# Optimization experiments

Measured on AMD Instinct MI355X. Metric: run time of the kernel, lower is better.

## Reference

```python
import jax, jax.numpy as jnp
import numpy as np

G = 16          # num graphs (equal-size contiguous segments)
P = 500         # kde_grid_points
Q = 20          # num quantiles, np.linspace(0,1,20)
SQRT2PI = float(np.sqrt(2.0 * np.pi))


def _gcn(x, src, dst, W, b):
    # PyG GCNConv: add self-loops, symmetric D^-1/2 (A+I) D^-1/2 aggregation.
    N = x.shape[0]
    xw = x @ W
    deg = jax.ops.segment_sum(jnp.ones_like(src, dtype=x.dtype), dst, num_segments=N) + 1.0
    dinv = jax.lax.rsqrt(deg)
    msg = xw[src] * (dinv[src] * dinv[dst])[:, None]            # [E, D]
    agg = jax.ops.segment_sum(msg, dst, num_segments=N) + xw * (dinv * dinv)[:, None]
    return agg + b


def _att_pool(x, Wg, bg):
    # GlobalAttention: softmax(gate_nn(x)) per graph, weighted sum of x.
    xg = x.reshape(G, -1, x.shape[-1])                          # [G, n, D]
    a = jax.nn.softmax(xg @ Wg + bg, axis=1)                    # [G, n, 1]
    return jnp.sum(a * xg, axis=1)                              # [G, D]


def _kde(xg):
    # xg: [n, D] nodes of one graph -> [D*Q] soft quantile features.
    quant = jnp.linspace(0.0, 1.0, Q, dtype=xg.dtype)
    n = xg.shape[0]
    mn = xg.min(axis=0) - 1e-6
    mx = xg.max(axis=0) + 1e-6
    grid = jnp.linspace(0.0, 1.0, P, dtype=xg.dtype)[:, None] * (mx - mn) + mn   # [P, D]
    std = xg.std(axis=0) + 1e-8 / 3                              # unbiased=False
    h = 1.06 * std * n ** (-0.2)                                 # Silverman bandwidth
    u = (grid[:, None, :] - xg[None, :, :]) / h                  # [P, n, D]
    kern = jnp.exp(-0.5 * u * u) / (h * SQRT2PI)
    dens = kern.mean(axis=1)                                     # [P, D]
    cdf = jnp.cumsum(dens, axis=0)
    cdf = cdf / jnp.clip(cdf[-1:], 1e-8)
    dist = jnp.abs(cdf[:, :, None] - quant)                      # [P, D, Q]
    w = jax.nn.sigmoid(-100.0 * dist)
    w = w / (w.sum(axis=0, keepdims=True) + 1e-8)
    return jnp.sum(grid[:, :, None] * w, axis=0).reshape(-1)     # [D*Q]


def setup_inputs() -> dict:
    key = jax.random.key(0)
    ks = jax.random.split(key, 26)
    N, E, D_in, D_h, D_out = 2048, 32768, 64, 64, 16
    rn = lambda k, s: jax.random.normal(k, s, jnp.float32) * 0.1
    return {
        'x': jax.random.normal(ks[0], (N, D_in), jnp.float32),
        'edge_index': jax.random.randint(ks[1], (2, E), 0, N),
        'gcn_W0': rn(ks[2], (D_in, D_h)), 'gcn_b0': rn(ks[3], (D_h,)),
        'gcn_W1': rn(ks[4], (D_h, D_h)), 'gcn_b1': rn(ks[5], (D_h,)),
        'lp_W0': rn(ks[6], (D_in, D_out)), 'lp_b0': rn(ks[7], (D_out,)),
        'lp_W1': rn(ks[8], (D_h, D_out)), 'lp_b1': rn(ks[9], (D_out,)),
        'cls_W': rn(ks[10], (D_h, D_out)), 'cls_b': rn(ks[11], (D_out,)),
        'kp_W0': rn(ks[12], (D_in * Q, D_out)), 'kp_b0': rn(ks[13], (D_out,)),
        'kp_W1': rn(ks[14], (D_h * Q, D_out)), 'kp_b1': rn(ks[15], (D_out,)),
        'gate_W0': rn(ks[16], (D_in, 1)), 'gate_b0': rn(ks[17], (1,)),
        'gate_W1': rn(ks[18], (D_h, 1)), 'gate_b1': rn(ks[19], (1,)),
        'gate_W2': rn(ks[20], (D_h, 1)), 'gate_b2': rn(ks[21], (1,)),
        'beta': jax.random.normal(ks[22], (D_out,), jnp.float32),
        'h0': jax.random.normal(ks[23], (1,), jnp.float32),
    }


def reference(x, edge_index, gcn_W0, gcn_b0, gcn_W1, gcn_b1, lp_W0, lp_b0, lp_W1, lp_b1,
              cls_W, cls_b, kp_W0, kp_b0, kp_W1, kp_b1, gate_W0, gate_b0, gate_W1, gate_b1,
              gate_W2, gate_b2, beta, h0):
    src, dst = edge_index[0], edge_index[1]
    gcn_p = [(gcn_W0, gcn_b0), (gcn_W1, gcn_b1)]
    lp = [(lp_W0, lp_b0), (lp_W1, lp_b1)]
    kp = [(kp_W0, kp_b0), (kp_W1, kp_b1)]
    gate = [(gate_W0, gate_b0), (gate_W1, gate_b1)]
    cur = x
    h_list, kde_list = [], []
    for i in range(2):  # n_layers (dropout is identity in eval)
        pooled = _att_pool(cur, *gate[i])                        # [G, D]
        h_list.append(pooled @ lp[i][0] + lp[i][1])              # [G, out]
        kf = jax.vmap(_kde)(cur.reshape(G, -1, cur.shape[-1]))   # [G, D*Q]
        kde_list.append(kf @ kp[i][0] + kp[i][1])
        cur = _gcn(cur, src, dst, *gcn_p[i])
    h_list.append(_att_pool(cur, gate_W2, gate_b2) @ cls_W + cls_b)
    main_out = jnp.stack(h_list).mean(axis=0)                    # [G, out]
    kde_out = jnp.stack(kde_list).mean(axis=0)
    return (main_out + kde_out) @ beta + h0                      # [G]
```

## Files before the change

kernel.cpp:

```cpp
#include <hip/hip_runtime.h>
#include <math.h>

#define NNODE 2048
#define NEDGE 32768
#define DD 64
#define GG 16
#define NPG 128
#define PP 500
#define QQ 20
#define CAP 64

__device__ __forceinline__ float fexp2(float x) { return __builtin_amdgcn_exp2f(x); }
__device__ __forceinline__ float frcp(float x)  { return __builtin_amdgcn_rcpf(x); }
__device__ __forceinline__ float frsq(float x)  { return __builtin_amdgcn_rsqf(x); }

struct __align__(8) f2 { float x, y; };

struct KdeS { f2 bc[NPG]; f2 cg[512]; float sred[8]; float wtot[8]; float kfv[QQ]; };
struct AttS { float sc[NPG]; float part[8][DD]; float pooled[DD]; };
struct XwS  { float Ws[DD][DD]; float xr[8][DD]; };
union SmemU { KdeS k; AttS a; XwS x; };

__global__ void k_zero(int* __restrict__ p) {
    p[blockIdx.x * 512 + threadIdx.x] = 0;
}

__global__ void k_fill(const int* __restrict__ ei, int* __restrict__ cnt,
                       int* __restrict__ csr) {
    int e = blockIdx.x * 256 + threadIdx.x;
    int s = ei[e], dstn = ei[NEDGE + e];
    int pos = atomicAdd(&cnt[dstn], 1);
    if (pos < CAP) csr[dstn * CAP + pos] = s;
}

__device__ __forceinline__ void att_pool(AttS& s, const float* __restrict__ xg,
                                         const float* __restrict__ gW, float gb) {
    int t = threadIdx.x, lane = t & 63, wid = t >> 6;
    int node = t >> 2, seg = t & 3;
    const float* row = xg + node * DD + seg * 16;
    const float* gw = gW + seg * 16;
    float v = 0.f;
    #pragma unroll
    for (int k = 0; k < 16; k++) v = fmaf(row[k], gw[k], v);
    v += __shfl_xor(v, 1);
    v += __shfl_xor(v, 2);
    if (seg == 0) s.sc[node] = v + gb;
    __syncthreads();
    if (wid == 0) {
        float v0 = s.sc[lane], v1 = s.sc[lane + 64];
        float m = fmaxf(v0, v1);
        for (int o = 32; o; o >>= 1) m = fmaxf(m, __shfl_xor(m, o));
        float e0 = __expf(v0 - m), e1 = __expf(v1 - m);
        float ssum = e0 + e1;
        for (int o = 32; o; o >>= 1) ssum += __shfl_xor(ssum, o);
        float inv = frcp(ssum);
        s.sc[lane] = e0 * inv;
        s.sc[lane + 64] = e1 * inv;
    }
    __syncthreads();
    int d2 = t & 63, ch = t >> 6;
    const float* base = xg + ch * 16 * DD + d2;
    const float* av = s.sc + ch * 16;
    float p = 0.f;
    #pragma unroll
    for (int i = 0; i < 16; i++) p = fmaf(av[i], base[i * DD], p);
    s.part[ch][d2] = p;
    __syncthreads();
    if (t < DD) {
        float pd = 0.f;
        #pragma unroll
        for (int c2 = 0; c2 < 8; c2++) pd += s.part[c2][t];
        s.pooled[t] = pd;
    }
    __syncthreads();
}

__global__ __launch_bounds__(512) void k_mega(
    const float* __restrict__ xin, const int* __restrict__ cnt,
    float* __restrict__ xwout, float* __restrict__ hb, float* __restrict__ kpart,
    const float* __restrict__ gcnW,
    const float* __restrict__ gateW, const float* __restrict__ gateB,
    const float* __restrict__ lpW, const float* __restrict__ lpB,
    const float* __restrict__ kpW) {
    __shared__ SmemU sm;
    int b = blockIdx.x, t = threadIdx.x, lane = t & 63, wid = t >> 6;

    if (b < GG * DD) {
        int g = b >> 6, d = b & 63;
        const float* xg = xin + g * NPG * DD + d;
        float a = 0.f;
        if (t < NPG) a = xg[t * DD];
        if (wid < 2) {
            float mn = a, mx = a, smv = a;
            for (int o = 32; o; o >>= 1) {
                mn = fminf(mn, __shfl_xor(mn, o));
                mx = fmaxf(mx, __shfl_xor(mx, o));
                smv += __shfl_xor(smv, o);
            }
            if (lane == 0) {
                sm.k.sred[wid * 3 + 0] = mn;
                sm.k.sred[wid * 3 + 1] = mx;
                sm.k.sred[wid * 3 + 2] = smv;
            }
        }
        __syncthreads();
        float mn = fminf(sm.k.sred[0], sm.k.sred[3]) - 1e-6f;
        float mx = fmaxf(sm.k.sred[1], sm.k.sred[4]) + 1e-6f;
        float mean = (sm.k.sred[2] + sm.k.sred[5]) * (1.f / 128.f);
        if (wid < 2) {
            float dv = a - mean;
            float sq = dv * dv;
            for (int o = 32; o; o >>= 1) sq += __shfl_xor(sq, o);
            if (lane == 0) sm.k.sred[6 + wid] = sq;
        }
        __syncthreads();
        float var = fmaxf((sm.k.sred[6] + sm.k.sred[7]) * (1.f / 128.f), 0.f);
        float sd = sqrtf(var) + (1e-8f / 3.0f);
        float h = 0.4016648901252554f * sd;
        const float L2E = 1.4426950408889634f;
        float A = -0.5f * L2E * frcp(h * h);
        if (t < NPG) { f2 v; v.x = -2.f * A * a; v.y = A * a * a; sm.k.bc[t] = v; }
        __syncthreads();
        float step = (mx - mn) * (1.f / 499.f);
        float gp = fmaf(step, (float)t, mn);
        float gA = A * gp * gp;
        const float4* bc4 = (const float4*)sm.k.bc;
        float ac0 = 0.f, ac1 = 0.f, ac2 = 0.f, ac3 = 0.f;
        #pragma unroll 4
        for (int j4 = 0; j4 < 64; j4 += 2) {
            float4 p = bc4[j4], q = bc4[j4 + 1];
            ac0 += fexp2(gA + fmaf(p.x, gp, p.y));
            ac1 += fexp2(gA + fmaf(p.z, gp, p.w));
            ac2 += fexp2(gA + fmaf(q.x, gp, q.y));
            ac3 += fexp2(gA + fmaf(q.z, gp, q.w));
        }
        float invnh = frcp(128.f * h * 2.5066282746310002f);
        float dens = (t < PP) ? ((ac0 + ac1) + (ac2 + ac3)) * invnh : 0.f;
        float sc2 = dens;
        for (int o = 1; o < 64; o <<= 1) {
            float u = __shfl_up(sc2, o);
            if (lane >= o) sc2 += u;
        }
        if (lane == 63) sm.k.wtot[wid] = sc2;
        __syncthreads();
        float offs = 0.f, total = 0.f;
        #pragma unroll
        for (int w = 0; w < 8; w++) {
            float wv = sm.k.wtot[w];
            if (w < wid) offs += wv;
            total += wv;
        }
        float c = (offs + sc2) * frcp(fmaxf(total, 1e-8f));
        f2 cgv; cgv.x = (t < PP) ? c : 4.0f; cgv.y = (t < PP) ? gp : 0.f;
        sm.k.cg[t] = cgv;
        __syncthreads();
        int grp = t >> 4, sub = t & 15;
        if (grp < QQ) {
            float qv = (float)grp * (1.f / 19.f);
            float sw0 = 0.f, sw1 = 0.f, sg0 = 0.f, sg1 = 0.f;
            #pragma unroll
            for (int i = 0; i < 32; i += 2) {
                f2 v0 = sm.k.cg[i * 16 + sub];
                f2 v1 = sm.k.cg[(i + 1) * 16 + sub];
                float e0 = fexp2(fabsf(v0.x - qv) * 144.26950408889634f);
                float e1 = fexp2(fabsf(v1.x - qv) * 144.26950408889634f);
                float w0 = frcp(1.f + e0), w1 = frcp(1.f + e1);
                sw0 += w0; sg0 = fmaf(w0, v0.y, sg0);
                sw1 += w1; sg1 = fmaf(w1, v1.y, sg1);
            }
            float sw = sw0 + sw1, sg = sg0 + sg1;
            #pragma unroll
            for (int o = 1; o < 16; o <<= 1) {
                sw += __shfl_xor(sw, o);
                sg += __shfl_xor(sg, o);
            }
            if (sub == 0) sm.k.kfv[grp] = sg * frcp(sw + 1e-8f);
        }
        __syncthreads();
        if (t < 16) {
            float v = 0.f;
            #pragma unroll
            for (int q = 0; q < QQ; q++) v = fmaf(sm.k.kfv[q], kpW[(d * QQ + q) * 16 + t], v);
            kpart[b * 16 + t] = v;
        }
    } else if (b < GG * DD + GG) {
        int g = b - GG * DD;
        att_pool(sm.a, xin + g * NPG * DD, gateW, gateB[0]);
        if (t < 16) {
            float o = lpB[t];
            #pragma unroll
            for (int d2 = 0; d2 < DD; d2++) o = fmaf(sm.a.pooled[d2], lpW[d2 * 16 + t], o);
            hb[g * 16 + t] = o;
        }
    } else {
        int rb = b - (GG * DD + GG);
        int r0 = rb * 8;
        float4* Wv = (float4*)&sm.x.Ws[0][0];
        const float4* Gv = (const float4*)gcnW;
        Wv[t] = Gv[t];
        Wv[t + 512] = Gv[t + 512];
        sm.x.xr[wid][lane] = xin[(r0 + wid) * DD + lane];
        __syncthreads();
        float s = 0.f;
        #pragma unroll
        for (int k = 0; k < DD; k++) s = fmaf(sm.x.xr[wid][k], sm.x.Ws[k][lane], s);
        float di = frsq((float)cnt[r0 + wid] + 1.0f);
        xwout[(r0 + wid) * DD + lane] = s * di;
    }
}

__global__ __launch_bounds__(512) void k_gather(const int* __restrict__ cnt,
                                                const int* __restrict__ csr,
                                                const float* __restrict__ xw,
                                                const float* __restrict__ bvec,
                                                float* __restrict__ cur) {
    int t = threadIdx.x, lane = t & 63, wid = t >> 6;
    int n = blockIdx.x * 8 + wid;
    int ec = cnt[n];
    if (ec > CAP) ec = CAP;
    const int* lst = csr + n * CAP;
    float sum0 = 0.f, sum1 = 0.f;
    int j = 0;
    for (; j + 4 <= ec; j += 4) {
        int s0 = lst[j], s1 = lst[j + 1], s2 = lst[j + 2], s3 = lst[j + 3];
        sum0 += xw[s0 * DD + lane] + xw[s1 * DD + lane];
        sum1 += xw[s2 * DD + lane] + xw[s3 * DD + lane];
    }
    for (; j < ec; j++) sum0 += xw[lst[j] * DD + lane];
    float di = frsq((float)cnt[n] + 1.f);
    cur[n * DD + lane] = di * ((sum0 + sum1) + xw[n * DD + lane]) + bvec[lane];
}

__global__ __launch_bounds__(512) void k_fin(const float* __restrict__ cur2,
    const float* __restrict__ gW2, const float* __restrict__ gb2,
    const float* __restrict__ clsW, const float* __restrict__ clsB,
    const float* __restrict__ hb, const float* __restrict__ kpart,
    const float* __restrict__ kpb0, const float* __restrict__ kpb1,
    const float* __restrict__ beta, const float* __restrict__ h0s,
    float* __restrict__ out) {
    __shared__ SmemU sm;
    __shared__ float red[16];
    int g = blockIdx.x, t = threadIdx.x;
    att_pool(sm.a, cur2 + g * NPG * DD, gW2, gb2[0]);
    if (t < 16) {
        float h2 = clsB[t];
        #pragma unroll
        for (int d2 = 0; d2 < DD; d2++) h2 = fmaf(sm.a.pooled[d2], clsW[d2 * 16 + t], h2);
        const float* kp0 = kpart + g * DD * 16 + t;
        const float* kp1 = kp0 + GG * DD * 16;
        float s0 = 0.f, s1 = 0.f;
        #pragma unroll
        for (int d2 = 0; d2 < DD; d2++) {
            s0 += kp0[d2 * 16];
            s1 += kp1[d2 * 16];
        }
        float mo = (hb[g * 16 + t] + hb[256 + g * 16 + t] + h2) * (1.f / 3.f);
        float ko = (s0 + kpb0[t] + s1 + kpb1[t]) * 0.5f;
        red[t] = (mo + ko) * beta[t];
    }
    __syncthreads();
    if (t == 0) {
        float s = 0.f;
        #pragma unroll
        for (int j = 0; j < 16; j++) s += red[j];
        out[g] = s + h0s[0];
    }
}

extern "C" void kernel_launch(void* const* d_in, const int* in_sizes, int n_in,
                              void* d_out, int out_size, void* d_ws, size_t ws_size,
                              hipStream_t stream) {
    const float* x       = (const float*)d_in[0];
    const int*   ei      = (const int*)  d_in[1];
    const float* gcn_W0  = (const float*)d_in[2];
    const float* gcn_b0  = (const float*)d_in[3];
    const float* gcn_W1  = (const float*)d_in[4];
    const float* gcn_b1  = (const float*)d_in[5];
    const float* lp_W0   = (const float*)d_in[6];
    const float* lp_b0   = (const float*)d_in[7];
    const float* lp_W1   = (const float*)d_in[8];
    const float* lp_b1   = (const float*)d_in[9];
    const float* cls_W   = (const float*)d_in[10];
    const float* cls_b   = (const float*)d_in[11];
    const float* kp_W0   = (const float*)d_in[12];
    const float* kp_b0   = (const float*)d_in[13];
    const float* kp_W1   = (const float*)d_in[14];
    const float* kp_b1   = (const float*)d_in[15];
    const float* gate_W0 = (const float*)d_in[16];
    const float* gate_b0 = (const float*)d_in[17];
    const float* gate_W1 = (const float*)d_in[18];
    const float* gate_b1 = (const float*)d_in[19];
    const float* gate_W2 = (const float*)d_in[20];
    const float* gate_b2 = (const float*)d_in[21];
    const float* beta    = (const float*)d_in[22];
    const float* h0s     = (const float*)d_in[23];

    float* ws  = (float*)d_ws;
    int* cnt   = (int*)ws;
    int* csr   = (int*)(ws + 2048);
    float* A   = ws + 2048 + NNODE * CAP;
    float* B   = A + NNODE * DD;
    float* hb  = B + NNODE * DD;
    float* kp  = hb + 512;

    k_zero<<<4, 512, 0, stream>>>(cnt);

    k_fill<<<NEDGE / 256, 256, 0, stream>>>(ei, cnt, csr);

    k_mega<<<GG * DD + GG + NNODE / 8, 512, 0, stream>>>(
        x, cnt, A, hb, kp, gcn_W0, gate_W0, gate_b0, lp_W0, lp_b0, kp_W0);
    k_gather<<<NNODE / 8, 512, 0, stream>>>(cnt, csr, A, gcn_b0, B);

    k_mega<<<GG * DD + GG + NNODE / 8, 512, 0, stream>>>(
        B, cnt, A, hb + 256, kp + GG * DD * 16, gcn_W1, gate_W1, gate_b1, lp_W1, lp_b1, kp_W1);
    k_gather<<<NNODE / 8, 512, 0, stream>>>(cnt, csr, A, gcn_b1, B);

    k_fin<<<GG, 512, 0, stream>>>(B, gate_W2, gate_b2, cls_W, cls_b,
                                  hb, kp, kp_b0, kp_b1, beta, h0s, (float*)d_out);
}
```

Before: 66.45 us.

## Fuse all stages into one persistent cooperative kernel with grid syncs

Replaces the seven separate launches (zero, CSR fill, two mega, two gather, final) with a single cooperative kernel of 256 blocks. Stages are separated by grid.sync, and one block builds the CSR while the other 255 run the layer-0 KDE, pooling and xW units. Because xW is now computed before the degree counts exist, the source-side degree scaling moves into the gather, which reads cnt[src] per edge. This removes launch gaps but serializes the CSR build onto one block and runs about six work units per block in the compute phases.

Result: slower. 241.1 us (+262.8%).

```diff
diff --git a/kernel.cpp b/kernel.cpp
--- a/kernel.cpp
+++ b/kernel.cpp
@@ -1,5 +1,8 @@
 #include <hip/hip_runtime.h>
+#include <hip/hip_cooperative_groups.h>
 #include <math.h>
+
+namespace cg = cooperative_groups;
 
 #define NNODE 2048
 #define NEDGE 32768
@@ -9,6 +12,8 @@
 #define PP 500
 #define QQ 20
 #define CAP 64
+#define NBLK 256
+#define NCOMP (NBLK - 1)
 
 __device__ __forceinline__ float fexp2(float x) { return __builtin_amdgcn_exp2f(x); }
 __device__ __forceinline__ float frcp(float x)  { return __builtin_amdgcn_rcpf(x); }
@@ -21,17 +26,17 @@
 struct XwS  { float Ws[DD][DD]; float xr[8][DD]; };
 union SmemU { KdeS k; AttS a; XwS x; };
 
-__global__ void k_zero(int* __restrict__ p) {
-    p[blockIdx.x * 512 + threadIdx.x] = 0;
-}
-
-__global__ void k_fill(const int* __restrict__ ei, int* __restrict__ cnt,
-                       int* __restrict__ csr) {
-    int e = blockIdx.x * 256 + threadIdx.x;
-    int s = ei[e], dstn = ei[NEDGE + e];
-    int pos = atomicAdd(&cnt[dstn], 1);
-    if (pos < CAP) csr[dstn * CAP + pos] = s;
-}
+struct Params {
+    const float *x; const int *ei;
+    const float *gcn_W0, *gcn_b0, *gcn_W1, *gcn_b1;
+    const float *lp_W0, *lp_b0, *lp_W1, *lp_b1;
+    const float *cls_W, *cls_b;
+    const float *kp_W0, *kp_b0, *kp_W1, *kp_b1;
+    const float *gate_W0, *gate_b0, *gate_W1, *gate_b1, *gate_W2, *gate_b2;
+    const float *beta, *h0s;
+    int *cnt, *csr;
+    float *A, *B, *hb, *kpart, *out;
+};
 
 __device__ __forceinline__ void att_pool(AttS& s, const float* __restrict__ xg,
                                          const float* __restrict__ gW, float gb) {
@@ -75,18 +80,18 @@
     __syncthreads();
 }
 
-__global__ __launch_bounds__(512) void k_mega(
-    const float* __restrict__ xin, const int* __restrict__ cnt,
-    float* __restrict__ xwout, float* __restrict__ hb, float* __restrict__ kpart,
+__device__ void mega_unit(SmemU& sm, int vb,
+    const float* __restrict__ xin,
+    float* __restrict__ xwout, float* __restrict__ hbL, float* __restrict__ kpartL,
     const float* __restrict__ gcnW,
     const float* __restrict__ gateW, const float* __restrict__ gateB,
     const float* __restrict__ lpW, const float* __restrict__ lpB,
     const float* __restrict__ kpW) {
-    __shared__ SmemU sm;
-    int b = blockIdx.x, t = threadIdx.x, lane = t & 63, wid = t >> 6;
-
-    if (b < GG * DD) {
-        int g = b >> 6, d = b & 63;
+    int t = threadIdx.x, lane = t & 63, wid = t >> 6;
+    __syncthreads();
+
+    if (vb < GG * DD) {
+        int g = vb >> 6, d = vb & 63;
         const float* xg = xin + g * NPG * DD + d;
         float a = 0.f;
         if (t < NPG) a = xg[t * DD];
@@ -117,8 +122,7 @@
         float var = fmaxf((sm.k.sred[6] + sm.k.sred[7]) * (1.f / 128.f), 0.f);
         float sd = sqrtf(var) + (1e-8f / 3.0f);
         float h = 0.4016648901252554f * sd;
-        const float L2E = 1.4426950408889634f;
-        float A = -0.5f * L2E * frcp(h * h);
+        float A = -0.5f * 1.4426950408889634f * frcp(h * h);
         if (t < NPG) { f2 v; v.x = -2.f * A * a; v.y = A * a * a; sm.k.bc[t] = v; }
         __syncthreads();
         float step = (mx - mn) * (1.f / 499.f);
@@ -181,19 +185,19 @@
             float v = 0.f;
             #pragma unroll
             for (int q = 0; q < QQ; q++) v = fmaf(sm.k.kfv[q], kpW[(d * QQ + q) * 16 + t], v);
-            kpart[b * 16 + t] = v;
-        }
-    } else if (b < GG * DD + GG) {
-        int g = b - GG * DD;
+            kpartL[vb * 16 + t] = v;
+        }
+    } else if (vb < GG * DD + GG) {
+        int g = vb - GG * DD;
         att_pool(sm.a, xin + g * NPG * DD, gateW, gateB[0]);
         if (t < 16) {
             float o = lpB[t];
             #pragma unroll
             for (int d2 = 0; d2 < DD; d2++) o = fmaf(sm.a.pooled[d2], lpW[d2 * 16 + t], o);
-            hb[g * 16 + t] = o;
+            hbL[g * 16 + t] = o;
         }
     } else {
-        int rb = b - (GG * DD + GG);
+        int rb = vb - (GG * DD + GG);
         int r0 = rb * 8;
         float4* Wv = (float4*)&sm.x.Ws[0][0];
         const float4* Gv = (const float4*)gcnW;
@@ -204,117 +208,144 @@
         float s = 0.f;
         #pragma unroll
         for (int k = 0; k < DD; k++) s = fmaf(sm.x.xr[wid][k], sm.x.Ws[k][lane], s);
-        float di = frsq((float)cnt[r0 + wid] + 1.0f);
-        xwout[(r0 + wid) * DD + lane] = s * di;
-    }
-}
-
-__global__ __launch_bounds__(512) void k_gather(const int* __restrict__ cnt,
-                                                const int* __restrict__ csr,
-                                                const float* __restrict__ xw,
-                                                const float* __restrict__ bvec,
-                                                float* __restrict__ cur) {
+        xwout[(r0 + wid) * DD + lane] = s;
+    }
+}
+
+__device__ void gather_unit(const int* __restrict__ cnt, const int* __restrict__ csr,
+                            const float* __restrict__ xw, const float* __restrict__ bvec,
+                            float* __restrict__ cur) {
     int t = threadIdx.x, lane = t & 63, wid = t >> 6;
     int n = blockIdx.x * 8 + wid;
-    int ec = cnt[n];
-    if (ec > CAP) ec = CAP;
+    int ecn = cnt[n];
+    int ec = ecn > CAP ? CAP : ecn;
     const int* lst = csr + n * CAP;
     float sum0 = 0.f, sum1 = 0.f;
     int j = 0;
-    for (; j + 4 <= ec; j += 4) {
-        int s0 = lst[j], s1 = lst[j + 1], s2 = lst[j + 2], s3 = lst[j + 3];
-        sum0 += xw[s0 * DD + lane] + xw[s1 * DD + lane];
-        sum1 += xw[s2 * DD + lane] + xw[s3 * DD + lane];
-    }
-    for (; j < ec; j++) sum0 += xw[lst[j] * DD + lane];
-    float di = frsq((float)cnt[n] + 1.f);
-    cur[n * DD + lane] = di * ((sum0 + sum1) + xw[n * DD + lane]) + bvec[lane];
-}
-
-__global__ __launch_bounds__(512) void k_fin(const float* __restrict__ cur2,
-    const float* __restrict__ gW2, const float* __restrict__ gb2,
-    const float* __restrict__ clsW, const float* __restrict__ clsB,
-    const float* __restrict__ hb, const float* __restrict__ kpart,
-    const float* __restrict__ kpb0, const float* __restrict__ kpb1,
-    const float* __restrict__ beta, const float* __restrict__ h0s,
-    float* __restrict__ out) {
+    for (; j + 2 <= ec; j += 2) {
+        int s0 = lst[j], s1 = lst[j + 1];
+        float d0 = frsq((float)cnt[s0] + 1.f);
+        float d1 = frsq((float)cnt[s1] + 1.f);
+        sum0 = fmaf(d0, xw[s0 * DD + lane], sum0);
+        sum1 = fmaf(d1, xw[s1 * DD + lane], sum1);
+    }
+    if (j < ec) {
+        int s0 = lst[j];
+        sum0 = fmaf(frsq((float)cnt[s0] + 1.f), xw[s0 * DD + lane], sum0);
+    }
+    float di = frsq((float)ecn + 1.f);
+    cur[n * DD + lane] = di * ((sum0 + sum1) + di * xw[n * DD + lane]) + bvec[lane];
+}
+
+__global__ __launch_bounds__(512) void k_all(Params p) {
     __shared__ SmemU sm;
     __shared__ float red[16];
-    int g = blockIdx.x, t = threadIdx.x;
-    att_pool(sm.a, cur2 + g * NPG * DD, gW2, gb2[0]);
-    if (t < 16) {
-        float h2 = clsB[t];
-        #pragma unroll
-        for (int d2 = 0; d2 < DD; d2++) h2 = fmaf(sm.a.pooled[d2], clsW[d2 * 16 + t], h2);
-        const float* kp0 = kpart + g * DD * 16 + t;
-        const float* kp1 = kp0 + GG * DD * 16;
-        float s0 = 0.f, s1 = 0.f;
-        #pragma unroll
-        for (int d2 = 0; d2 < DD; d2++) {
-            s0 += kp0[d2 * 16];
-            s1 += kp1[d2 * 16];
-        }
-        float mo = (hb[g * 16 + t] + hb[256 + g * 16 + t] + h2) * (1.f / 3.f);
-        float ko = (s0 + kpb0[t] + s1 + kpb1[t]) * 0.5f;
-        red[t] = (mo + ko) * beta[t];
-    }
-    __syncthreads();
-    if (t == 0) {
-        float s = 0.f;
-        #pragma unroll
-        for (int j = 0; j < 16; j++) s += red[j];
-        out[g] = s + h0s[0];
+    cg::grid_group grid = cg::this_grid();
+    int b = blockIdx.x, t = threadIdx.x;
+
+    if (b == NCOMP) {
+        for (int i = t; i < NNODE; i += 512) p.cnt[i] = 0;
+        __syncthreads();
+        for (int e = t; e < NEDGE; e += 512) {
+            int s = p.ei[e], dstn = p.ei[NEDGE + e];
+            int pos = atomicAdd(&p.cnt[dstn], 1);
+            if (pos < CAP) p.csr[dstn * CAP + pos] = s;
+        }
+    } else {
+        #pragma unroll
+        for (int k = 0; k < 6; k++) {
+            int vb = b + NCOMP * k;
+            if (vb < GG * DD + GG + NNODE / 8)
+                mega_unit(sm, vb, p.x, p.A, p.hb, p.kpart,
+                          p.gcn_W0, p.gate_W0, p.gate_b0, p.lp_W0, p.lp_b0, p.kp_W0);
+        }
+    }
+    grid.sync();
+
+    gather_unit(p.cnt, p.csr, p.A, p.gcn_b0, p.B);
+    grid.sync();
+
+    if (b < NCOMP) {
+        #pragma unroll
+        for (int k = 0; k < 6; k++) {
+            int vb = b + NCOMP * k;
+            if (vb < GG * DD + GG + NNODE / 8)
+                mega_unit(sm, vb, p.B, p.A, p.hb + 256, p.kpart + GG * DD * 16,
+                          p.gcn_W1, p.gate_W1, p.gate_b1, p.lp_W1, p.lp_b1, p.kp_W1);
+        }
+    }
+    grid.sync();
+
+    gather_unit(p.cnt, p.csr, p.A, p.gcn_b1, p.B);
+    grid.sync();
+
+    if (b < GG) {
+        int g = b;
+        att_pool(sm.a, p.B + g * NPG * DD, p.gate_W2, p.gate_b2[0]);
+        if (t < 16) {
+            float h2 = p.cls_b[t];
+            #pragma unroll
+            for (int d2 = 0; d2 < DD; d2++) h2 = fmaf(sm.a.pooled[d2], p.cls_W[d2 * 16 + t], h2);
+            const float* kp0 = p.kpart + g * DD * 16 + t;
+            const float* kp1 = kp0 + GG * DD * 16;
+            float s0 = 0.f, s1 = 0.f;
+            #pragma unroll
+            for (int d2 = 0; d2 < DD; d2++) {
+                s0 += kp0[d2 * 16];
+                s1 += kp1[d2 * 16];
+            }
+            float mo = (p.hb[g * 16 + t] + p.hb[256 + g * 16 + t] + h2) * (1.f / 3.f);
+            float ko = (s0 + p.kp_b0[t] + s1 + p.kp_b1[t]) * 0.5f;
+            red[t] = (mo + ko) * p.beta[t];
+        }
+        __syncthreads();
+        if (t == 0) {
+            float s = 0.f;
+            #pragma unroll
+            for (int j = 0; j < 16; j++) s += red[j];
+            p.out[g] = s + p.h0s[0];
+        }
     }
 }
 
 extern "C" void kernel_launch(void* const* d_in, const int* in_sizes, int n_in,
                               void* d_out, int out_size, void* d_ws, size_t ws_size,
                               hipStream_t stream) {
-    const float* x       = (const float*)d_in[0];
-    const int*   ei      = (const int*)  d_in[1];
-    const float* gcn_W0  = (const float*)d_in[2];
-    const float* gcn_b0  = (const float*)d_in[3];
-    const float* gcn_W1  = (const float*)d_in[4];
-    const float* gcn_b1  = (const float*)d_in[5];
-    const float* lp_W0   = (const float*)d_in[6];
-    const float* lp_b0   = (const float*)d_in[7];
-    const float* lp_W1   = (const float*)d_in[8];
-    const float* lp_b1   = (const float*)d_in[9];
-    const float* cls_W   = (const float*)d_in[10];
-    const float* cls_b   = (const float*)d_in[11];
-    const float* kp_W0   = (const float*)d_in[12];
-    const float* kp_b0   = (const float*)d_in[13];
-    const float* kp_W1   = (const float*)d_in[14];
-    const float* kp_b1   = (const float*)d_in[15];
-    const float* gate_W0 = (const float*)d_in[16];
-    const float* gate_b0 = (const float*)d_in[17];
-    const float* gate_W1 = (const float*)d_in[18];
-    const float* gate_b1 = (const float*)d_in[19];
-    const float* gate_W2 = (const float*)d_in[20];
-    const float* gate_b2 = (const float*)d_in[21];
-    const float* beta    = (const float*)d_in[22];
-    const float* h0s     = (const float*)d_in[23];
-
-    float* ws  = (float*)d_ws;
-    int* cnt   = (int*)ws;
-    int* csr   = (int*)(ws + 2048);
-    float* A   = ws + 2048 + NNODE * CAP;
-    float* B   = A + NNODE * DD;
-    float* hb  = B + NNODE * DD;
-    float* kp  = hb + 512;
-
-    k_zero<<<4, 512, 0, stream>>>(cnt);
-
-    k_fill<<<NEDGE / 256, 256, 0, stream>>>(ei, cnt, csr);
-
-    k_mega<<<GG * DD + GG + NNODE / 8, 512, 0, stream>>>(
-        x, cnt, A, hb, kp, gcn_W0, gate_W0, gate_b0, lp_W0, lp_b0, kp_W0);
-    k_gather<<<NNODE / 8, 512, 0, stream>>>(cnt, csr, A, gcn_b0, B);
-
-    k_mega<<<GG * DD + GG + NNODE / 8, 512, 0, stream>>>(
-        B, cnt, A, hb + 256, kp + GG * DD * 16, gcn_W1, gate_W1, gate_b1, lp_W1, lp_b1, kp_W1);
-    k_gather<<<NNODE / 8, 512, 0, stream>>>(cnt, csr, A, gcn_b1, B);
-
-    k_fin<<<GG, 512, 0, stream>>>(B, gate_W2, gate_b2, cls_W, cls_b,
-                                  hb, kp, kp_b0, kp_b1, beta, h0s, (float*)d_out);
-}
+    Params hp;
+    hp.x       = (const float*)d_in[0];
+    hp.ei      = (const int*)  d_in[1];
+    hp.gcn_W0  = (const float*)d_in[2];
+    hp.gcn_b0  = (const float*)d_in[3];
+    hp.gcn_W1  = (const float*)d_in[4];
+    hp.gcn_b1  = (const float*)d_in[5];
+    hp.lp_W0   = (const float*)d_in[6];
+    hp.lp_b0   = (const float*)d_in[7];
+    hp.lp_W1   = (const float*)d_in[8];
+    hp.lp_b1   = (const float*)d_in[9];
+    hp.cls_W   = (const float*)d_in[10];
+    hp.cls_b   = (const float*)d_in[11];
+    hp.kp_W0   = (const float*)d_in[12];
+    hp.kp_b0   = (const float*)d_in[13];
+    hp.kp_W1   = (const float*)d_in[14];
+    hp.kp_b1   = (const float*)d_in[15];
+    hp.gate_W0 = (const float*)d_in[16];
+    hp.gate_b0 = (const float*)d_in[17];
+    hp.gate_W1 = (const float*)d_in[18];
+    hp.gate_b1 = (const float*)d_in[19];
+    hp.gate_W2 = (const float*)d_in[20];
+    hp.gate_b2 = (const float*)d_in[21];
+    hp.beta    = (const float*)d_in[22];
+    hp.h0s     = (const float*)d_in[23];
+
+    float* ws = (float*)d_ws;
+    hp.cnt   = (int*)ws;
+    hp.csr   = hp.cnt + NNODE;
+    hp.A     = (float*)(hp.csr + NNODE * CAP);
+    hp.B     = hp.A + NNODE * DD;
+    hp.hb    = hp.B + NNODE * DD;
+    hp.kpart = hp.hb + 512;
+    hp.out   = (float*)d_out;
+
+    void* args[] = { &hp };
+    hipLaunchCooperativeKernel((void*)k_all, dim3(NBLK), dim3(512), args, 0, stream);
+}
```

## Fold CSR build into first mega kernel and fuse final gather with pooling

Applied to the files above, without the earlier changes.

The CSR build now runs as an extra block of the first k_mega launch, using a shared-memory count array, so the separate zero and fill kernels go away. Source-side degree normalization moves from the xw GEMM into the gather, so xw no longer depends on the edge counts and can be computed concurrently with CSR construction. The second gather is fused into the final kernel: each of 16 blocks aggregates its graph's 128 nodes into shared memory, then does attention pooling and the kpart reduction there. This removes three launches, but the CSR block is a single serial block over 32768 edges and the final gather runs on only 16 blocks, so either could lengthen the critical path.

New measurement: 151.4 us. 2.28x slower.

```diff
diff --git a/kernel.cpp b/kernel.cpp
--- a/kernel.cpp
+++ b/kernel.cpp
@@ -19,74 +19,22 @@
 struct KdeS { f2 bc[NPG]; f2 cg[512]; float sred[8]; float wtot[8]; float kfv[QQ]; };
 struct AttS { float sc[NPG]; float part[8][DD]; float pooled[DD]; };
 struct XwS  { float Ws[DD][DD]; float xr[8][DD]; };
-union SmemU { KdeS k; AttS a; XwS x; };
-
-__global__ void k_zero(int* __restrict__ p) {
-    p[blockIdx.x * 512 + threadIdx.x] = 0;
-}
-
-__global__ void k_fill(const int* __restrict__ ei, int* __restrict__ cnt,
-                       int* __restrict__ csr) {
-    int e = blockIdx.x * 256 + threadIdx.x;
-    int s = ei[e], dstn = ei[NEDGE + e];
-    int pos = atomicAdd(&cnt[dstn], 1);
-    if (pos < CAP) csr[dstn * CAP + pos] = s;
-}
-
-__device__ __forceinline__ void att_pool(AttS& s, const float* __restrict__ xg,
-                                         const float* __restrict__ gW, float gb) {
-    int t = threadIdx.x, lane = t & 63, wid = t >> 6;
-    int node = t >> 2, seg = t & 3;
-    const float* row = xg + node * DD + seg * 16;
-    const float* gw = gW + seg * 16;
-    float v = 0.f;
-    #pragma unroll
-    for (int k = 0; k < 16; k++) v = fmaf(row[k], gw[k], v);
-    v += __shfl_xor(v, 1);
-    v += __shfl_xor(v, 2);
-    if (seg == 0) s.sc[node] = v + gb;
-    __syncthreads();
-    if (wid == 0) {
-        float v0 = s.sc[lane], v1 = s.sc[lane + 64];
-        float m = fmaxf(v0, v1);
-        for (int o = 32; o; o >>= 1) m = fmaxf(m, __shfl_xor(m, o));
-        float e0 = __expf(v0 - m), e1 = __expf(v1 - m);
-        float ssum = e0 + e1;
-        for (int o = 32; o; o >>= 1) ssum += __shfl_xor(ssum, o);
-        float inv = frcp(ssum);
-        s.sc[lane] = e0 * inv;
-        s.sc[lane + 64] = e1 * inv;
-    }
-    __syncthreads();
-    int d2 = t & 63, ch = t >> 6;
-    const float* base = xg + ch * 16 * DD + d2;
-    const float* av = s.sc + ch * 16;
-    float p = 0.f;
-    #pragma unroll
-    for (int i = 0; i < 16; i++) p = fmaf(av[i], base[i * DD], p);
-    s.part[ch][d2] = p;
-    __syncthreads();
-    if (t < DD) {
-        float pd = 0.f;
-        #pragma unroll
-        for (int c2 = 0; c2 < 8; c2++) pd += s.part[c2][t];
-        s.pooled[t] = pd;
-    }
-    __syncthreads();
-}
+struct CsrS { int cnti[NNODE]; };
+union SmemU { KdeS k; AttS a; XwS x; CsrS c; };
 
 __global__ __launch_bounds__(512) void k_mega(
-    const float* __restrict__ xin, const int* __restrict__ cnt,
-    float* __restrict__ xwout, float* __restrict__ hb, float* __restrict__ kpart,
+    const float* __restrict__ xin, const int* __restrict__ ei,
+    int* __restrict__ cnt, int* __restrict__ csr,
+    float* __restrict__ xwout, float* __restrict__ hbL, float* __restrict__ kpartL,
     const float* __restrict__ gcnW,
     const float* __restrict__ gateW, const float* __restrict__ gateB,
     const float* __restrict__ lpW, const float* __restrict__ lpB,
     const float* __restrict__ kpW) {
     __shared__ SmemU sm;
-    int b = blockIdx.x, t = threadIdx.x, lane = t & 63, wid = t >> 6;
-
-    if (b < GG * DD) {
-        int g = b >> 6, d = b & 63;
+    int vb = blockIdx.x, t = threadIdx.x, lane = t & 63, wid = t >> 6;
+
+    if (vb < GG * DD) {
+        int g = vb >> 6, d = vb & 63;
         const float* xg = xin + g * NPG * DD + d;
         float a = 0.f;
         if (t < NPG) a = xg[t * DD];
@@ -117,8 +65,7 @@
         float var = fmaxf((sm.k.sred[6] + sm.k.sred[7]) * (1.f / 128.f), 0.f);
         float sd = sqrtf(var) + (1e-8f / 3.0f);
         float h = 0.4016648901252554f * sd;
-        const float L2E = 1.4426950408889634f;
-        float A = -0.5f * L2E * frcp(h * h);
+        float A = -0.5f * 1.4426950408889634f * frcp(h * h);
         if (t < NPG) { f2 v; v.x = -2.f * A * a; v.y = A * a * a; sm.k.bc[t] = v; }
         __syncthreads();
         float step = (mx - mn) * (1.f / 499.f);
@@ -181,19 +128,56 @@
             float v = 0.f;
             #pragma unroll
             for (int q = 0; q < QQ; q++) v = fmaf(sm.k.kfv[q], kpW[(d * QQ + q) * 16 + t], v);
-            kpart[b * 16 + t] = v;
-        }
-    } else if (b < GG * DD + GG) {
-        int g = b - GG * DD;
-        att_pool(sm.a, xin + g * NPG * DD, gateW, gateB[0]);
+            kpartL[vb * 16 + t] = v;
+        }
+    } else if (vb < GG * DD + GG) {
+        int g = vb - GG * DD;
+        const float* xg = xin + g * NPG * DD;
+        int node = t >> 2, seg = t & 3;
+        const float* row = xg + node * DD + seg * 16;
+        const float* gw = gateW + seg * 16;
+        float v = 0.f;
+        #pragma unroll
+        for (int k = 0; k < 16; k++) v = fmaf(row[k], gw[k], v);
+        v += __shfl_xor(v, 1);
+        v += __shfl_xor(v, 2);
+        if (seg == 0) sm.a.sc[node] = v + gateB[0];
+        __syncthreads();
+        if (wid == 0) {
+            float v0 = sm.a.sc[lane], v1 = sm.a.sc[lane + 64];
+            float m = fmaxf(v0, v1);
+            for (int o = 32; o; o >>= 1) m = fmaxf(m, __shfl_xor(m, o));
+            float e0 = __expf(v0 - m), e1 = __expf(v1 - m);
+            float ssum = e0 + e1;
+            for (int o = 32; o; o >>= 1) ssum += __shfl_xor(ssum, o);
+            float inv = frcp(ssum);
+            sm.a.sc[lane] = e0 * inv;
+            sm.a.sc[lane + 64] = e1 * inv;
+        }
+        __syncthreads();
+        int d2 = t & 63, ch = t >> 6;
+        const float* base = xg + ch * 16 * DD + d2;
+        const float* av = sm.a.sc + ch * 16;
+        float p = 0.f;
+        #pragma unroll
+        for (int i = 0; i < 16; i++) p = fmaf(av[i], base[i * DD], p);
+        sm.a.part[ch][d2] = p;
+        __syncthreads();
+        if (t < DD) {
+            float pd = 0.f;
+            #pragma unroll
+            for (int c2 = 0; c2 < 8; c2++) pd += sm.a.part[c2][t];
+            sm.a.pooled[t] = pd;
+        }
+        __syncthreads();
         if (t < 16) {
             float o = lpB[t];
             #pragma unroll
-            for (int d2 = 0; d2 < DD; d2++) o = fmaf(sm.a.pooled[d2], lpW[d2 * 16 + t], o);
-            hb[g * 16 + t] = o;
-        }
-    } else {
-        int rb = b - (GG * DD + GG);
+            for (int d2_ = 0; d2_ < DD; d2_++) o = fmaf(sm.a.pooled[d2_], lpW[d2_ * 16 + t], o);
+            hbL[g * 16 + t] = o;
+        }
+    } else if (vb < GG * DD + GG + NNODE / 8) {
+        int rb = vb - (GG * DD + GG);
         int r0 = rb * 8;
         float4* Wv = (float4*)&sm.x.Ws[0][0];
         const float4* Gv = (const float4*)gcnW;
@@ -204,8 +188,18 @@
         float s = 0.f;
         #pragma unroll
         for (int k = 0; k < DD; k++) s = fmaf(sm.x.xr[wid][k], sm.x.Ws[k][lane], s);
-        float di = frsq((float)cnt[r0 + wid] + 1.0f);
-        xwout[(r0 + wid) * DD + lane] = s * di;
+        xwout[(r0 + wid) * DD + lane] = s;
+    } else {
+        int* cl = sm.c.cnti;
+        for (int i = t; i < NNODE; i += 512) cl[i] = 0;
+        __syncthreads();
+        for (int e = t; e < NEDGE; e += 512) {
+            int s = ei[e], dstn = ei[NEDGE + e];
+            int pos = atomicAdd(&cl[dstn], 1);
+            if (pos < CAP) csr[dstn * CAP + pos] = s;
+        }
+        __syncthreads();
+        for (int i = t; i < NNODE; i += 512) cnt[i] = cl[i];
     }
 }
 
@@ -216,46 +210,115 @@
                                                 float* __restrict__ cur) {
     int t = threadIdx.x, lane = t & 63, wid = t >> 6;
     int n = blockIdx.x * 8 + wid;
-    int ec = cnt[n];
-    if (ec > CAP) ec = CAP;
+    int ecn = cnt[n];
+    int ec = ecn > CAP ? CAP : ecn;
     const int* lst = csr + n * CAP;
     float sum0 = 0.f, sum1 = 0.f;
     int j = 0;
-    for (; j + 4 <= ec; j += 4) {
-        int s0 = lst[j], s1 = lst[j + 1], s2 = lst[j + 2], s3 = lst[j + 3];
-        sum0 += xw[s0 * DD + lane] + xw[s1 * DD + lane];
-        sum1 += xw[s2 * DD + lane] + xw[s3 * DD + lane];
-    }
-    for (; j < ec; j++) sum0 += xw[lst[j] * DD + lane];
-    float di = frsq((float)cnt[n] + 1.f);
-    cur[n * DD + lane] = di * ((sum0 + sum1) + xw[n * DD + lane]) + bvec[lane];
+    for (; j + 2 <= ec; j += 2) {
+        int s0 = lst[j], s1 = lst[j + 1];
+        sum0 = fmaf(frsq((float)cnt[s0] + 1.f), xw[s0 * DD + lane], sum0);
+        sum1 = fmaf(frsq((float)cnt[s1] + 1.f), xw[s1 * DD + lane], sum1);
+    }
+    if (j < ec) {
+        int s0 = lst[j];
+        sum0 = fmaf(frsq((float)cnt[s0] + 1.f), xw[s0 * DD + lane], sum0);
+    }
+    float di = frsq((float)ecn + 1.f);
+    cur[n * DD + lane] = di * ((sum0 + sum1) + di * xw[n * DD + lane]) + bvec[lane];
 }
 
-__global__ __launch_bounds__(512) void k_fin(const float* __restrict__ cur2,
+__global__ __launch_bounds__(512) void k_gfin(
+    const int* __restrict__ cnt, const int* __restrict__ csr,
+    const float* __restrict__ xw, const float* __restrict__ gcn_b1,
     const float* __restrict__ gW2, const float* __restrict__ gb2,
     const float* __restrict__ clsW, const float* __restrict__ clsB,
     const float* __restrict__ hb, const float* __restrict__ kpart,
     const float* __restrict__ kpb0, const float* __restrict__ kpb1,
     const float* __restrict__ beta, const float* __restrict__ h0s,
     float* __restrict__ out) {
-    __shared__ SmemU sm;
+    __shared__ float xs[NPG][DD];
+    __shared__ AttS sa;
+    __shared__ float red2[32][16];
     __shared__ float red[16];
-    int g = blockIdx.x, t = threadIdx.x;
-    att_pool(sm.a, cur2 + g * NPG * DD, gW2, gb2[0]);
+    int g = blockIdx.x, t = threadIdx.x, lane = t & 63, wid = t >> 6;
+
+    for (int i = 0; i < 16; i++) {
+        int nl = wid * 16 + i;
+        int n = g * NPG + nl;
+        int ecn = cnt[n];
+        int ec = ecn > CAP ? CAP : ecn;
+        const int* lst = csr + n * CAP;
+        float s0 = 0.f, s1 = 0.f;
+        int j = 0;
+        for (; j + 2 <= ec; j += 2) {
+            int a0 = lst[j], a1 = lst[j + 1];
+            s0 = fmaf(frsq((float)cnt[a0] + 1.f), xw[a0 * DD + lane], s0);
+            s1 = fmaf(frsq((float)cnt[a1] + 1.f), xw[a1 * DD + lane], s1);
+        }
+        if (j < ec) {
+            int a0 = lst[j];
+            s0 = fmaf(frsq((float)cnt[a0] + 1.f), xw[a0 * DD + lane], s0);
+        }
+        float di = frsq((float)ecn + 1.f);
+        xs[nl][lane] = di * ((s0 + s1) + di * xw[n * DD + lane]) + gcn_b1[lane];
+    }
+    __syncthreads();
+
+    int node = t >> 2, seg = t & 3;
+    const float* gw = gW2 + seg * 16;
+    float v = 0.f;
+    #pragma unroll
+    for (int k = 0; k < 16; k++) v = fmaf(xs[node][seg * 16 + k], gw[k], v);
+    v += __shfl_xor(v, 1);
+    v += __shfl_xor(v, 2);
+    if (seg == 0) sa.sc[node] = v + gb2[0];
+    __syncthreads();
+    if (wid == 0) {
+        float v0 = sa.sc[lane], v1 = sa.sc[lane + 64];
+        float m = fmaxf(v0, v1);
+        for (int o = 32; o; o >>= 1) m = fmaxf(m, __shfl_xor(m, o));
+        float e0 = __expf(v0 - m), e1 = __expf(v1 - m);
+        float ssum = e0 + e1;
+        for (int o = 32; o; o >>= 1) ssum += __shfl_xor(ssum, o);
+        float inv = frcp(ssum);
+        sa.sc[lane] = e0 * inv;
+        sa.sc[lane + 64] = e1 * inv;
+    }
+    __syncthreads();
+    int d2 = t & 63, ch = t >> 6;
+    float p = 0.f;
+    #pragma unroll
+    for (int i = 0; i < 16; i++) p = fmaf(sa.sc[ch * 16 + i], xs[ch * 16 + i][d2], p);
+    sa.part[ch][d2] = p;
+    __syncthreads();
+    if (t < DD) {
+        float pd = 0.f;
+        #pragma unroll
+        for (int c2 = 0; c2 < 8; c2++) pd += sa.part[c2][t];
+        sa.pooled[t] = pd;
+    }
+    {
+        int j = t & 15, u = t >> 4;
+        int L = u >> 4, dg = u & 15;
+        float s = 0.f;
+        #pragma unroll
+        for (int dd2 = 0; dd2 < 4; dd2++) {
+            int d = dg * 4 + dd2;
+            s += kpart[(L * GG * DD + g * DD + d) * 16 + j];
+        }
+        red2[u][j] = s;
+    }
+    __syncthreads();
     if (t < 16) {
+        float sk = 0.f;
+        #pragma unroll
+        for (int u2 = 0; u2 < 32; u2++) sk += red2[u2][t];
         float h2 = clsB[t];
         #pragma unroll
-        for (int d2 = 0; d2 < DD; d2++) h2 = fmaf(sm.a.pooled[d2], clsW[d2 * 16 + t], h2);
-        const float* kp0 = kpart + g * DD * 16 + t;
-        const float* kp1 = kp0 + GG * DD * 16;
-        float s0 = 0.f, s1 = 0.f;
-        #pragma unroll
-        for (int d2 = 0; d2 < DD; d2++) {
-            s0 += kp0[d2 * 16];
-            s1 += kp1[d2 * 16];
-        }
+        for (int d3 = 0; d3 < DD; d3++) h2 = fmaf(sa.pooled[d3], clsW[d3 * 16 + t], h2);
         float mo = (hb[g * 16 + t] + hb[256 + g * 16 + t] + h2) * (1.f / 3.f);
-        float ko = (s0 + kpb0[t] + s1 + kpb1[t]) * 0.5f;
+        float ko = (sk + kpb0[t] + kpb1[t]) * 0.5f;
         red[t] = (mo + ko) * beta[t];
     }
     __syncthreads();
@@ -295,26 +358,27 @@
     const float* beta    = (const float*)d_in[22];
     const float* h0s     = (const float*)d_in[23];
 
-    float* ws  = (float*)d_ws;
+    float* ws = (float*)d_ws;
     int* cnt   = (int*)ws;
-    int* csr   = (int*)(ws + 2048);
-    float* A   = ws + 2048 + NNODE * CAP;
+    int* csr   = cnt + NNODE;
+    float* A   = (float*)(csr + NNODE * CAP);
     float* B   = A + NNODE * DD;
     float* hb  = B + NNODE * DD;
     float* kp  = hb + 512;
 
-    k_zero<<<4, 512, 0, stream>>>(cnt);
-
-    k_fill<<<NEDGE / 256, 256, 0, stream>>>(ei, cnt, csr);
-
-    k_mega<<<GG * DD + GG + NNODE / 8, 512, 0, stream>>>(
-        x, cnt, A, hb, kp, gcn_W0, gate_W0, gate_b0, lp_W0, lp_b0, kp_W0);
+    const int NMEGA = GG * DD + GG + NNODE / 8;
+
+    k_mega<<<NMEGA + 1, 512, 0, stream>>>(
+        x, ei, cnt, csr, A, hb, kp,
+        gcn_W0, gate_W0, gate_b0, lp_W0, lp_b0, kp_W0);
+
     k_gather<<<NNODE / 8, 512, 0, stream>>>(cnt, csr, A, gcn_b0, B);
 
-    k_mega<<<GG * DD + GG + NNODE / 8, 512, 0, stream>>>(
-        B, cnt, A, hb + 256, kp + GG * DD * 16, gcn_W1, gate_W1, gate_b1, lp_W1, lp_b1, kp_W1);
-    k_gather<<<NNODE / 8, 512, 0, stream>>>(cnt, csr, A, gcn_b1, B);
-
-    k_fin<<<GG, 512, 0, stream>>>(B, gate_W2, gate_b2, cls_W, cls_b,
-                                  hb, kp, kp_b0, kp_b1, beta, h0s, (float*)d_out);
+    k_mega<<<NMEGA, 512, 0, stream>>>(
+        B, ei, cnt, csr, A, hb + 256, kp + GG * DD * 16,
+        gcn_W1, gate_W1, gate_b1, lp_W1, lp_b1, kp_W1);
+
+    k_gfin<<<GG, 512, 0, stream>>>(cnt, csr, A, gcn_b1,
+                                   gate_W2, gate_b2, cls_W, cls_b,
+                                   hb, kp, kp_b0, kp_b1, beta, h0s, (float*)d_out);
 }
```
